# Optimization experiments

Hardware: AMD Instinct MI355X
Metric: run time of the kernel (lower is better)

The kernel has to match this reference:

```python
import jax, jax.numpy as jnp
from jax import lax
import numpy as np

NUM_TIMESTEPS = 5
ALPHA = 0.9      # membrane decay
THRESHOLD = 1.0  # spike threshold


@jax.custom_vjp
def spike(v):
    # Heaviside spike with SuperSpike surrogate gradient (defined in vjp rules).
    return (v > 0.0).astype(v.dtype)

def _spike_fwd(v):
    return spike(v), v

def _spike_bwd(v, g):
    beta = 10.0
    sg = 1.0 / (1.0 + beta * jnp.abs(v)) ** 2
    return (g * sg,)

spike.defvjp(_spike_fwd, _spike_bwd)


def setup_inputs() -> dict:
    key = jax.random.key(0)
    B, S, I, H = 16, 64, 128, 512
    x = jax.random.normal(key, (B, S, I, H), dtype=jnp.float32)
    encoding = jnp.ones((I, H), dtype=jnp.float32)  # reset_parameters: fill_(1.0)
    return {"x": x, "encoding": encoding}


def reference(x, encoding):
    # x: [B, S, I, H], encoding: [I, H]
    B, S, I, H = x.shape
    # i = sum(encoding * x, dim=2) -> [B, S, H]
    cur = jnp.einsum("bsih,ih->bsh", x, encoding)
    # Each sequence position drives the dynamics for NUM_TIMESTEPS steps.
    cur_rep = jnp.repeat(cur, NUM_TIMESTEPS, axis=1)          # [B, S*T, H]
    cur_tb = jnp.moveaxis(cur_rep, 1, 0)                       # [S*T, B, H]

    def step(v, i_t):
        v = ALPHA * v + i_t
        z = spike(v - THRESHOLD)
        v = v - z * THRESHOLD  # soft reset
        return v, z

    v0 = jnp.zeros((B, H), dtype=x.dtype)
    _, zs = lax.scan(step, v0, cur_tb)                         # zs: [S*T, B, H]
    return jnp.moveaxis(zs, 0, 1)                              # [B, S*T, H]
```

## Files before the change

### kernel.cpp

```cpp
#include <hip/hip_runtime.h>

#define BB 16
#define SS 64
#define II 128
#define HH 512
#define TT 5
#define ALPHA 0.9f
#define THRESH 1.0f

__global__ __launch_bounds__(256) void einsum_kernel(const float4* __restrict__ x,
                                                     const float4* __restrict__ enc,
                                                     float4* __restrict__ cur) {
    const int H4 = HH / 4;
    int tid = blockIdx.x * blockDim.x + threadIdx.x;
    int h4 = tid & (H4 - 1);
    int bs = tid >> 7;
    const float4* xp = x + (size_t)bs * (II * H4) + h4;
    float4 acc = make_float4(0.f, 0.f, 0.f, 0.f);
#pragma unroll 8
    for (int i = 0; i < II; ++i) {
        float4 xv = xp[(size_t)i * H4];
        float4 ev = enc[i * H4 + h4];
        acc.x = fmaf(xv.x, ev.x, acc.x);
        acc.y = fmaf(xv.y, ev.y, acc.y);
        acc.z = fmaf(xv.z, ev.z, acc.z);
        acc.w = fmaf(xv.w, ev.w, acc.w);
    }
    cur[tid] = acc;
}

__global__ __launch_bounds__(64) void scan_kernel(const float* __restrict__ cur,
                                                  float* __restrict__ out) {
    int tid = blockIdx.x * blockDim.x + threadIdx.x;
    int h = tid & (HH - 1);
    int b = tid >> 9;
    const float* cp = cur + (size_t)b * SS * HH + h;
    float* op = out + (size_t)b * (SS * TT) * HH + h;
    float v = 0.f;
    for (int s = 0; s < SS; ++s) {
        float it = cp[(size_t)s * HH];
#pragma unroll
        for (int t = 0; t < TT; ++t) {
            v = ALPHA * v + it;
            float z = (v > THRESH) ? 1.0f : 0.0f;
            op[(size_t)(s * TT + t) * HH] = z;
            v -= z;
        }
    }
}

extern "C" void kernel_launch(void* const* d_in, const int* in_sizes, int n_in,
                              void* d_out, int out_size, void* d_ws, size_t ws_size,
                              hipStream_t stream) {
    const float* x   = (const float*)d_in[0];
    const float* enc = (const float*)d_in[1];
    float* out = (float*)d_out;
    float* cur = (float*)d_ws;

    einsum_kernel<<<512, 256, 0, stream>>>((const float4*)x, (const float4*)enc,
                                           (float4*)cur);
    scan_kernel<<<128, 64, 0, stream>>>(cur, out);
}
```

Before: 372.9 us.

## Vectorize scan to float4 per thread, add prefetch and nontemporal loads/stores

The scan kernel now has each thread handle four hidden units with float4 loads and nontemporal float4 stores, and it prefetches the input current two steps ahead. The grid shrinks from 128 to 32 blocks of 64 threads. The einsum kernel uses nontemporal loads for x and a deeper unroll. The goal is to cut per-element memory instruction overhead and latency stalls in the serial scan. In exchange, only 2048 threads run the scan, which lowers parallelism on a large GPU.

```diff
diff --git a/kernel.cpp b/kernel.cpp
--- a/kernel.cpp
+++ b/kernel.cpp
@@ -8,19 +8,22 @@
 #define ALPHA 0.9f
 #define THRESH 1.0f
 
-__global__ __launch_bounds__(256) void einsum_kernel(const float4* __restrict__ x,
-                                                     const float4* __restrict__ enc,
-                                                     float4* __restrict__ cur) {
+typedef float v4f __attribute__((ext_vector_type(4)));
+
+__global__ __launch_bounds__(256) void einsum_kernel(const v4f* __restrict__ x,
+                                                     const v4f* __restrict__ enc,
+                                                     v4f* __restrict__ cur) {
     const int H4 = HH / 4;
     int tid = blockIdx.x * blockDim.x + threadIdx.x;
     int h4 = tid & (H4 - 1);
     int bs = tid >> 7;
-    const float4* xp = x + (size_t)bs * (II * H4) + h4;
-    float4 acc = make_float4(0.f, 0.f, 0.f, 0.f);
-#pragma unroll 8
+    const v4f* xp = x + (size_t)bs * (II * H4) + h4;
+    const v4f* ep = enc + h4;
+    v4f acc = (v4f)(0.f);
+#pragma unroll 16
     for (int i = 0; i < II; ++i) {
-        float4 xv = xp[(size_t)i * H4];
-        float4 ev = enc[i * H4 + h4];
+        v4f xv = __builtin_nontemporal_load(&xp[(size_t)i * H4]);
+        v4f ev = ep[(size_t)i * H4];
         acc.x = fmaf(xv.x, ev.x, acc.x);
         acc.y = fmaf(xv.y, ev.y, acc.y);
         acc.z = fmaf(xv.z, ev.z, acc.z);
@@ -29,22 +32,36 @@
     cur[tid] = acc;
 }
 
-__global__ __launch_bounds__(64) void scan_kernel(const float* __restrict__ cur,
-                                                  float* __restrict__ out) {
+__global__ __launch_bounds__(64) void scan_kernel(const v4f* __restrict__ cur,
+                                                  v4f* __restrict__ out) {
+    const int H4 = HH / 4;
     int tid = blockIdx.x * blockDim.x + threadIdx.x;
-    int h = tid & (HH - 1);
-    int b = tid >> 9;
-    const float* cp = cur + (size_t)b * SS * HH + h;
-    float* op = out + (size_t)b * (SS * TT) * HH + h;
-    float v = 0.f;
+    int h4 = tid & (H4 - 1);
+    int b = tid >> 7;
+    const v4f* cp = cur + (size_t)b * SS * H4 + h4;
+    v4f* op = out + (size_t)b * (SS * TT) * H4 + h4;
+
+    v4f v = (v4f)(0.f);
+    v4f it0 = cp[0];
+    v4f it1 = cp[H4];
     for (int s = 0; s < SS; ++s) {
-        float it = cp[(size_t)s * HH];
+        v4f it = it0;
+        it0 = it1;
+        if (s + 2 < SS) it1 = cp[(size_t)(s + 2) * H4];
+        v4f* o = op + (size_t)s * TT * H4;
 #pragma unroll
         for (int t = 0; t < TT; ++t) {
-            v = ALPHA * v + it;
-            float z = (v > THRESH) ? 1.0f : 0.0f;
-            op[(size_t)(s * TT + t) * HH] = z;
-            v -= z;
+            v.x = fmaf(ALPHA, v.x, it.x);
+            v.y = fmaf(ALPHA, v.y, it.y);
+            v.z = fmaf(ALPHA, v.z, it.z);
+            v.w = fmaf(ALPHA, v.w, it.w);
+            v4f z;
+            z.x = (v.x > THRESH) ? 1.0f : 0.0f;
+            z.y = (v.y > THRESH) ? 1.0f : 0.0f;
+            z.z = (v.z > THRESH) ? 1.0f : 0.0f;
+            z.w = (v.w > THRESH) ? 1.0f : 0.0f;
+            v.x -= z.x;  v.y -= z.y;  v.z -= z.z;  v.w -= z.w;
+            __builtin_nontemporal_store(z, &o[(size_t)t * H4]);
         }
     }
 }
@@ -57,7 +74,7 @@
     float* out = (float*)d_out;
     float* cur = (float*)d_ws;
 
-    einsum_kernel<<<512, 256, 0, stream>>>((const float4*)x, (const float4*)enc,
-                                           (float4*)cur);
-    scan_kernel<<<128, 64, 0, stream>>>(cur, out);
+    einsum_kernel<<<512, 256, 0, stream>>>((const v4f*)x, (const v4f*)enc,
+                                           (v4f*)cur);
+    scan_kernel<<<32, 64, 0, stream>>>((const v4f*)cur, (v4f*)out);
 }
```

After: 367.3 us. No clear change (-1.5%).
